# Performance work log

Measured on AMD Instinct MI355X. Metric: run time of the kernel, lower is better.

The kernel has to match this reference:

```python
import jax, jax.numpy as jnp
import numpy as np

INPUT_DIM = 256
HIDDEN_DIM = 64
BATCH = 1024
N_ITEMS = 200


def setup_inputs() -> dict:
    key = jax.random.key(0)
    k1, k2, k3, k4, k5 = jax.random.split(key, 5)
    item_embedding = jax.random.normal(k1, (BATCH, N_ITEMS, INPUT_DIM), dtype=jnp.float32)
    query_embedding = jax.random.normal(k2, (BATCH, INPUT_DIM), dtype=jnp.float32)
    # query_projection: Linear(input_dim -> input_dim*hidden_dim); xavier-ish scale
    W_q = jax.random.normal(k3, (INPUT_DIM, INPUT_DIM * HIDDEN_DIM), dtype=jnp.float32) * 0.02
    b_q = jax.random.uniform(k4, (INPUT_DIM * HIDDEN_DIM,), dtype=jnp.float32, minval=0.0, maxval=0.01)
    # reduce_projection: Linear(hidden_dim -> 1, bias=False)
    W_r = jax.random.normal(k5, (HIDDEN_DIM,), dtype=jnp.float32) * 0.1
    return {
        "item_embedding": item_embedding,
        "query_embedding": query_embedding,
        "W_q": W_q,
        "b_q": b_q,
        "W_r": W_r,
    }


def reference(item_embedding, query_embedding, W_q, b_q, W_r):
    B = query_embedding.shape[0]
    # linear + tanh, reshape to (B, input_dim, hidden_dim)
    projected_query = jnp.tanh(query_embedding @ W_q + b_q)
    projected_query = projected_query.reshape(B, INPUT_DIM, HIDDEN_DIM)
    # batched einsum: (B, R, I) x (B, I, H) -> (B, R, H)
    dotted = jnp.einsum('bri,bih->brh', item_embedding, projected_query)
    # reduce_projection (H -> 1, no bias): score (B, R)
    score = jnp.einsum('brh,h->br', dotted, W_r)
    # ZAM normalization: exp / (1 + sum exp) over items
    es = jnp.exp(score)
    weight = es / (1.0 + jnp.sum(es, axis=1, keepdims=True))  # (B, R)
    # weighted sum over items -> (B, input_dim)
    entity_embedding = jnp.einsum('br,bri->bi', weight, item_embedding)
    return entity_embedding
```

## Files before the change

kernel.cpp:

```cpp
#include <hip/hip_runtime.h>

#define IDIM   256
#define HDIM   64
#define BATCH  1024
#define NITEMS 200
#define NCOLS  (IDIM * HDIM)

typedef __bf16 bf16x8 __attribute__((ext_vector_type(8)));
typedef float  f32x4  __attribute__((ext_vector_type(4)));

__device__ __forceinline__ unsigned short f2bf(float f) {
    unsigned int u = __float_as_uint(f);
    u += 0x7FFFu + ((u >> 16) & 1u);
    return (unsigned short)(u >> 16);
}

__device__ __forceinline__ float fast_tanh(float x) {
    float e2 = __expf(2.0f * x);
    return 1.0f - 2.0f * __builtin_amdgcn_rcpf(e2 + 1.0f);
}

__global__ __launch_bounds__(256) void k_conv_q(const float* __restrict__ q,
                                                unsigned short* __restrict__ Aq) {
    int idx = blockIdx.x * 256 + threadIdx.x;
    float4 f = ((const float4*)q)[idx];
    ushort4 o;
    o.x = f2bf(f.x); o.y = f2bf(f.y); o.z = f2bf(f.z); o.w = f2bf(f.w);
    ((ushort4*)Aq)[idx] = o;
}

__global__ __launch_bounds__(256) void k_trans_wq(const float* __restrict__ Wq,
                                                  unsigned short* __restrict__ Bt) {
    __shared__ float tile[32][33];
    int n0 = blockIdx.x * 32;
    int k0 = blockIdx.y * 32;
    int tx = threadIdx.x & 31;
    int ty = threadIdx.x >> 5;
#pragma unroll
    for (int j = 0; j < 32; j += 8)
        tile[ty + j][tx] = Wq[(size_t)(k0 + ty + j) * NCOLS + n0 + tx];
    __syncthreads();
#pragma unroll
    for (int j = 0; j < 32; j += 8)
        Bt[(size_t)(n0 + ty + j) * IDIM + k0 + tx] = f2bf(tile[tx][ty + j]);
}

__global__ __launch_bounds__(256) void k_gemm_v(const unsigned short* __restrict__ Aq,
                                                const unsigned short* __restrict__ Bt,
                                                const float* __restrict__ bq,
                                                const float* __restrict__ Wr,
                                                float* __restrict__ V) {
    int w    = threadIdx.x >> 6;
    int lane = threadIdx.x & 63;
    int l16  = lane & 15;
    int quad = lane >> 4;
    int blk  = blockIdx.x;
    int bn   = blk & 127;
    int bm   = blk >> 7;
    int m_tile = bm * 2 + (w & 1);
    int n_tile = bn * 2 + (w >> 1);
    int m_base = m_tile * 64;
    int n_base = n_tile * 64;

    f32x4 acc[4][4] = {};
    const unsigned short* Ap = Aq + (size_t)(m_base + l16) * IDIM + quad * 8;
    const unsigned short* Bp = Bt + (size_t)(n_base + l16) * IDIM + quad * 8;

    float bv[4], wr[4];
#pragma unroll
    for (int nt = 0; nt < 4; nt++) {
        int nl = nt * 16 + l16;
        bv[nt] = bq[n_base + nl];
        wr[nt] = Wr[nl];
    }

#pragma unroll
    for (int k0 = 0; k0 < IDIM; k0 += 32) {
        bf16x8 a[4], b[4];
#pragma unroll
        for (int t = 0; t < 4; t++) a[t] = *(const bf16x8*)(Ap + (size_t)t * 16 * IDIM + k0);
#pragma unroll
        for (int t = 0; t < 4; t++) b[t] = *(const bf16x8*)(Bp + (size_t)t * 16 * IDIM + k0);
#pragma unroll
        for (int mt = 0; mt < 4; mt++)
#pragma unroll
            for (int nt = 0; nt < 4; nt++)
                acc[mt][nt] = __builtin_amdgcn_mfma_f32_16x16x32_bf16(a[mt], b[nt], acc[mt][nt], 0, 0, 0);
    }

    int i = n_tile;
#pragma unroll
    for (int mt = 0; mt < 4; mt++) {
#pragma unroll
        for (int reg = 0; reg < 4; reg++) {
            float s = 0.0f;
#pragma unroll
            for (int nt = 0; nt < 4; nt++) {
                float c = acc[mt][nt][reg] + bv[nt];
                s += fast_tanh(c) * wr[nt];
            }
            s += __shfl_xor(s, 1);
            s += __shfl_xor(s, 2);
            s += __shfl_xor(s, 4);
            s += __shfl_xor(s, 8);
            if (l16 == 0) {
                int m = m_base + mt * 16 + quad * 4 + reg;
                V[m * IDIM + i] = s;
            }
        }
    }
}

__global__ __launch_bounds__(256) void k_score(const float* __restrict__ item,
                                               const float* __restrict__ V,
                                               float* __restrict__ out) {
    __shared__ float lacc[16][IDIM];
    __shared__ float lS[16];
    int b    = blockIdx.x;
    int tid  = threadIdx.x;
    int wid  = tid >> 6;
    int lane = tid & 63;
    int l16  = lane & 15;
    int quad = lane >> 4;

    const float4* itemB = (const float4*)(item + (size_t)b * NITEMS * IDIM);
    const float4* Vb    = (const float4*)(V + (size_t)b * IDIM);

    float4 v[4];
#pragma unroll
    for (int c = 0; c < 4; c++) v[c] = Vb[l16 + 16 * c];

    float4 acc[4];
#pragma unroll
    for (int c = 0; c < 4; c++) acc[c] = make_float4(0.f, 0.f, 0.f, 0.f);
    float S = 0.f;

    for (int chunk = wid; chunk < 25; chunk += 4) {
        int r0 = chunk * 8 + quad;
        int r1 = r0 + 4;
        float4 x0[4], x1[4];
#pragma unroll
        for (int c = 0; c < 4; c++) x0[c] = itemB[(size_t)r0 * 64 + l16 + 16 * c];
#pragma unroll
        for (int c = 0; c < 4; c++) x1[c] = itemB[(size_t)r1 * 64 + l16 + 16 * c];

        float d0 = 0.f, d1 = 0.f;
#pragma unroll
        for (int c = 0; c < 4; c++) {
            d0 += x0[c].x * v[c].x + x0[c].y * v[c].y + x0[c].z * v[c].z + x0[c].w * v[c].w;
            d1 += x1[c].x * v[c].x + x1[c].y * v[c].y + x1[c].z * v[c].z + x1[c].w * v[c].w;
        }
#pragma unroll
        for (int m = 1; m < 16; m <<= 1) {
            d0 += __shfl_xor(d0, m);
            d1 += __shfl_xor(d1, m);
        }
        float e0 = __expf(d0);
        float e1 = __expf(d1);
        S += e0 + e1;
#pragma unroll
        for (int c = 0; c < 4; c++) {
            acc[c].x += e0 * x0[c].x + e1 * x1[c].x;
            acc[c].y += e0 * x0[c].y + e1 * x1[c].y;
            acc[c].z += e0 * x0[c].z + e1 * x1[c].z;
            acc[c].w += e0 * x0[c].w + e1 * x1[c].w;
        }
    }

    int row = wid * 4 + quad;
#pragma unroll
    for (int c = 0; c < 4; c++)
        ((float4*)&lacc[row][0])[l16 + 16 * c] = acc[c];
    if (l16 == 0) lS[row] = S;
    __syncthreads();

    float s = 0.f;
#pragma unroll
    for (int i = 0; i < 16; i++) s += lacc[i][tid];
    float Stot = 0.f;
#pragma unroll
    for (int i = 0; i < 16; i++) Stot += lS[i];
    out[(size_t)b * IDIM + tid] = s / (1.0f + Stot);
}

extern "C" void kernel_launch(void* const* d_in, const int* in_sizes, int n_in,
                              void* d_out, int out_size, void* d_ws, size_t ws_size,
                              hipStream_t stream) {
    const float* item  = (const float*)d_in[0];
    const float* query = (const float*)d_in[1];
    const float* Wq    = (const float*)d_in[2];
    const float* bq    = (const float*)d_in[3];
    const float* Wr    = (const float*)d_in[4];
    float* out = (float*)d_out;

    char* ws = (char*)d_ws;
    unsigned short* Aq = (unsigned short*)ws;
    unsigned short* Bt = (unsigned short*)(ws + (512 << 10));
    float*          V  = (float*)(ws + (512 << 10) + (8 << 20));

    k_conv_q  <<<256,             256, 0, stream>>>(query, Aq);
    k_trans_wq<<<dim3(512, 8),    256, 0, stream>>>(Wq, Bt);
    k_gemm_v  <<<1024,            256, 0, stream>>>(Aq, Bt, bq, Wr, V);
    k_score   <<<1024,            256, 0, stream>>>(item, V, out);
}
```

Measured before the change: 344.5 us.

## Stage GEMM tiles in LDS via direct global-to-LDS loads and merge prep kernels

The q-conversion and Wq-transpose kernels become one launch, which removes one kernel launch. The GEMM block now cooperatively loads 128x32 A and B tiles into shared memory with global_load_lds, and its four waves share them instead of each wave reading its own 64-row slices from global memory. Each wave then reads its fragments from LDS. This cuts redundant global/L2 traffic at the cost of two barriers per k-step and no double buffering.

```diff
diff --git a/kernel.cpp b/kernel.cpp
--- a/kernel.cpp
+++ b/kernel.cpp
@@ -20,22 +20,29 @@
     return 1.0f - 2.0f * __builtin_amdgcn_rcpf(e2 + 1.0f);
 }
 
-__global__ __launch_bounds__(256) void k_conv_q(const float* __restrict__ q,
-                                                unsigned short* __restrict__ Aq) {
-    int idx = blockIdx.x * 256 + threadIdx.x;
-    float4 f = ((const float4*)q)[idx];
-    ushort4 o;
-    o.x = f2bf(f.x); o.y = f2bf(f.y); o.z = f2bf(f.z); o.w = f2bf(f.w);
-    ((ushort4*)Aq)[idx] = o;
-}
-
-__global__ __launch_bounds__(256) void k_trans_wq(const float* __restrict__ Wq,
-                                                  unsigned short* __restrict__ Bt) {
+#define GLOAD_LDS16(g, l) __builtin_amdgcn_global_load_lds(                 \
+    (const __attribute__((address_space(1))) void*)(g),                     \
+    (__attribute__((address_space(3))) void*)(l), 16, 0, 0)
+
+__global__ __launch_bounds__(256) void k_prep(const float* __restrict__ q,
+                                              const float* __restrict__ Wq,
+                                              unsigned short* __restrict__ Aq,
+                                              unsigned short* __restrict__ Bt) {
     __shared__ float tile[32][33];
-    int n0 = blockIdx.x * 32;
-    int k0 = blockIdx.y * 32;
-    int tx = threadIdx.x & 31;
-    int ty = threadIdx.x >> 5;
+    int blk = blockIdx.x;
+    int tid = threadIdx.x;
+    if (blk >= 4096) {
+        int idx = (blk - 4096) * 256 + tid;
+        float4 f = ((const float4*)q)[idx];
+        ushort4 o;
+        o.x = f2bf(f.x); o.y = f2bf(f.y); o.z = f2bf(f.z); o.w = f2bf(f.w);
+        ((ushort4*)Aq)[idx] = o;
+        return;
+    }
+    int n0 = (blk & 511) * 32;
+    int k0 = (blk >> 9) * 32;
+    int tx = tid & 31;
+    int ty = tid >> 5;
 #pragma unroll
     for (int j = 0; j < 32; j += 8)
         tile[ty + j][tx] = Wq[(size_t)(k0 + ty + j) * NCOLS + n0 + tx];
@@ -50,21 +57,29 @@
                                                 const float* __restrict__ bq,
                                                 const float* __restrict__ Wr,
                                                 float* __restrict__ V) {
-    int w    = threadIdx.x >> 6;
-    int lane = threadIdx.x & 63;
+    __shared__ __align__(16) unsigned short As[128 * 32];
+    __shared__ __align__(16) unsigned short Bs[128 * 32];
+    int tid  = threadIdx.x;
+    int w    = tid >> 6;
+    int lane = tid & 63;
     int l16  = lane & 15;
     int quad = lane >> 4;
     int blk  = blockIdx.x;
     int bn   = blk & 127;
     int bm   = blk >> 7;
-    int m_tile = bm * 2 + (w & 1);
-    int n_tile = bn * 2 + (w >> 1);
-    int m_base = m_tile * 64;
-    int n_base = n_tile * 64;
-
-    f32x4 acc[4][4] = {};
-    const unsigned short* Ap = Aq + (size_t)(m_base + l16) * IDIM + quad * 8;
-    const unsigned short* Bp = Bt + (size_t)(n_base + l16) * IDIM + quad * 8;
+
+    int m_off  = (w & 1) * 64;
+    int n_off  = (w >> 1) * 64;
+    int n_base = bn * 128 + n_off;
+    int icol   = bn * 2 + (w >> 1);
+
+    const unsigned short* Ag = Aq + (size_t)(bm * 128 + (tid >> 2)) * IDIM + (tid & 3) * 8;
+    const unsigned short* Bg = Bt + (size_t)(bn * 128 + (tid >> 2)) * IDIM + (tid & 3) * 8;
+    unsigned short* Asl = As + tid * 8;
+    unsigned short* Bsl = Bs + tid * 8;
+
+    const unsigned short* Asp = As + (m_off + l16) * 32 + quad * 8;
+    const unsigned short* Bsp = Bs + (n_off + l16) * 32 + quad * 8;
 
     float bv[4], wr[4];
 #pragma unroll
@@ -74,21 +89,27 @@
         wr[nt] = Wr[nl];
     }
 
-#pragma unroll
-    for (int k0 = 0; k0 < IDIM; k0 += 32) {
+    f32x4 acc[4][4] = {};
+#pragma unroll
+    for (int kk = 0; kk < IDIM; kk += 32) {
+        GLOAD_LDS16(Ag + kk,             Asl);
+        GLOAD_LDS16(Ag + 64 * IDIM + kk, Asl + 2048);
+        GLOAD_LDS16(Bg + kk,             Bsl);
+        GLOAD_LDS16(Bg + 64 * IDIM + kk, Bsl + 2048);
+        __syncthreads();
         bf16x8 a[4], b[4];
 #pragma unroll
-        for (int t = 0; t < 4; t++) a[t] = *(const bf16x8*)(Ap + (size_t)t * 16 * IDIM + k0);
-#pragma unroll
-        for (int t = 0; t < 4; t++) b[t] = *(const bf16x8*)(Bp + (size_t)t * 16 * IDIM + k0);
+        for (int t = 0; t < 4; t++) a[t] = *(const bf16x8*)(Asp + t * 16 * 32);
+#pragma unroll
+        for (int t = 0; t < 4; t++) b[t] = *(const bf16x8*)(Bsp + t * 16 * 32);
 #pragma unroll
         for (int mt = 0; mt < 4; mt++)
 #pragma unroll
             for (int nt = 0; nt < 4; nt++)
                 acc[mt][nt] = __builtin_amdgcn_mfma_f32_16x16x32_bf16(a[mt], b[nt], acc[mt][nt], 0, 0, 0);
-    }
-
-    int i = n_tile;
+        __syncthreads();
+    }
+
 #pragma unroll
     for (int mt = 0; mt < 4; mt++) {
 #pragma unroll
@@ -104,8 +125,8 @@
             s += __shfl_xor(s, 4);
             s += __shfl_xor(s, 8);
             if (l16 == 0) {
-                int m = m_base + mt * 16 + quad * 4 + reg;
-                V[m * IDIM + i] = s;
+                int m = bm * 128 + m_off + mt * 16 + quad * 4 + reg;
+                V[m * IDIM + icol] = s;
             }
         }
     }
@@ -198,8 +219,7 @@
     unsigned short* Bt = (unsigned short*)(ws + (512 << 10));
     float*          V  = (float*)(ws + (512 << 10) + (8 << 20));
 
-    k_conv_q  <<<256,             256, 0, stream>>>(query, Aq);
-    k_trans_wq<<<dim3(512, 8),    256, 0, stream>>>(Wq, Bt);
-    k_gemm_v  <<<1024,            256, 0, stream>>>(Aq, Bt, bq, Wr, V);
-    k_score   <<<1024,            256, 0, stream>>>(item, V, out);
-}
+    k_prep  <<<4352, 256, 0, stream>>>(query, Wq, Aq, Bt);
+    k_gemm_v<<<1024, 256, 0, stream>>>(Aq, Bt, bq, Wr, V);
+    k_score <<<1024, 256, 0, stream>>>(item, V, out);
+}
```

After: 328.5 us. -4.6%, faster.
